# Kernel tuning notes

Hardware: AMD Instinct MI355X
Metric: run time of the kernel (lower is better)

## Reference

```python
import jax, jax.numpy as jnp
import numpy as np

T, D, E, I, TOP_K = 4096, 2048, 8, 4096, 2

def setup_inputs() -> dict:
    key = jax.random.key(0)
    k1, k2, k3, k4, k5 = jax.random.split(key, 5)
    s = 0.02
    return {
        "hidden_states": jax.random.normal(k1, (T, D), jnp.float32),
        "wr": jax.random.normal(k2, (E, D), jnp.float32) * s,
        "w1": jax.random.normal(k3, (E, I, D), jnp.float32) * s,
        "v1": jax.random.normal(k4, (E, I, D), jnp.float32) * s,
        "w2": jax.random.normal(k5, (E, D, I), jnp.float32) * s,
        "index": 0,
    }

def reference(hidden_states, wr, w1, v1, w2, index):
    # index selects the layer; n_layers == 1 here so weights are already that layer's.
    x = hidden_states.reshape(-1, D)  # [T, D]
    # Router logits + softmax top-k with renormalization (fused_moe semantics)
    logits = x @ wr.T                                  # [T, E]
    probs = jax.nn.softmax(logits, axis=-1)
    topw, topi = jax.lax.top_k(probs, TOP_K)           # [T, K]
    topw = topw / jnp.sum(topw, axis=-1, keepdims=True)
    # Dense per-token gate matrix, zero for non-selected experts
    t_idx = jnp.arange(x.shape[0])[:, None]
    gates = jnp.zeros((x.shape[0], E), x.dtype).at[t_idx, topi].set(topw)  # [T, E]
    # SiLU-GLU experts: (silu(x w1^T) * (x v1^T)) w2^T, combined by gates
    out = jnp.zeros_like(x)
    for e in range(E):  # fixed small expert count
        h = jax.nn.silu(x @ w1[e].T) * (x @ v1[e].T)   # [T, I]
        out = out + gates[:, e:e + 1] * (h @ w2[e].T)  # [T, D]
    return out
```

## Files before the change

### kernel.cpp

```cpp
#include <hip/hip_runtime.h>
#include <hip/hip_bf16.h>
#include <cstdint>


#define T_TOK 4096
#define DHID  2048
#define NEXP  8
#define IDIM  4096
#define NSLOT (T_TOK * 2)

#define BM 128
#define BN 128
#define BK 64

typedef __bf16 bf16x8 __attribute__((ext_vector_type(8)));
typedef float  f32x4  __attribute__((ext_vector_type(4)));

__global__ __launch_bounds__(64) void router_kernel(
    const float* __restrict__ x, const float* __restrict__ wr,
    __bf16* __restrict__ xb, int* __restrict__ topi, float* __restrict__ topg,
    int* __restrict__ cnt)
{
    int t = blockIdx.x;
    int lane = threadIdx.x;
    const float* xr = x + (size_t)t * DHID;
    float acc[NEXP];
#pragma unroll
    for (int e = 0; e < NEXP; ++e) acc[e] = 0.f;
    for (int j = 0; j < DHID / 64; ++j) {
        int d = lane + j * 64;
        float xv = xr[d];
        xb[(size_t)t * DHID + d] = (__bf16)xv;
#pragma unroll
        for (int e = 0; e < NEXP; ++e) acc[e] += xv * wr[e * DHID + d];
    }
#pragma unroll
    for (int e = 0; e < NEXP; ++e) {
#pragma unroll
        for (int s = 32; s > 0; s >>= 1) acc[e] += __shfl_xor(acc[e], s);
    }
    if (lane == 0) {
        int e0 = 0; float l0 = acc[0];
#pragma unroll
        for (int e = 1; e < NEXP; ++e) if (acc[e] > l0) { l0 = acc[e]; e0 = e; }
        int e1 = -1; float l1 = -3.4e38f;
#pragma unroll
        for (int e = 0; e < NEXP; ++e) if (e != e0 && acc[e] > l1) { l1 = acc[e]; e1 = e; }
        float g0 = 1.f / (1.f + __expf(l1 - l0));
        topi[t * 2]     = e0; topi[t * 2 + 1] = e1;
        topg[t * 2]     = g0; topg[t * 2 + 1] = 1.f - g0;
        atomicAdd(&cnt[e0], 1); atomicAdd(&cnt[e1], 1);
    }
}

__global__ void scan_kernel(const int* __restrict__ cnt, int* __restrict__ basep,
                            int* __restrict__ fill)
{
    if (threadIdx.x == 0 && blockIdx.x == 0) {
        int s = 0;
#pragma unroll
        for (int e = 0; e < NEXP; ++e) { basep[e] = s; s += cnt[e]; fill[e] = 0; }
    }
}

__global__ __launch_bounds__(256) void assign_kernel(
    const int* __restrict__ topi, const float* __restrict__ topg,
    const int* __restrict__ basep, int* __restrict__ fill,
    int* __restrict__ tok_of_slot, float* __restrict__ gate_of_slot,
    int* __restrict__ slot_of)
{
    int t = blockIdx.x * 256 + threadIdx.x;
    if (t >= T_TOK) return;
#pragma unroll
    for (int k = 0; k < 2; ++k) {
        int e = topi[t * 2 + k];
        int slot = basep[e] + atomicAdd(&fill[e], 1);
        tok_of_slot[slot] = t;
        gate_of_slot[slot] = topg[t * 2 + k];
        slot_of[t * 2 + k] = slot;
    }
}

__global__ __launch_bounds__(256, 2) void gemm1_kernel(
    const __bf16* __restrict__ xb, const float* __restrict__ w1,
    const float* __restrict__ v1, const int* __restrict__ tok_of_slot,
    const int* __restrict__ cnt, const int* __restrict__ basep,
    __bf16* __restrict__ H)
{
    int e  = blockIdx.z;
    int ne = cnt[e];
    int m0 = blockIdx.y * BM;
    if (m0 >= ne) return;
    int n0 = blockIdx.x * BN;
    int sbase = basep[e] + m0;

    __shared__ __bf16 As[BM * BK];
    __shared__ __bf16 B1s[BN * BK];
    __shared__ __bf16 B2s[BN * BK];
    __shared__ int toks[BM];

    int tid = threadIdx.x;
    if (tid < BM) {
        int t = 0;
        if (m0 + tid < ne) t = tok_of_slot[sbase + tid];
        toks[tid] = t;
    }
    __syncthreads();

    const float* w1e = w1 + (size_t)e * IDIM * DHID;
    const float* v1e = v1 + (size_t)e * IDIM * DHID;

    int lane = tid & 63;
    int wave = tid >> 6;
    int wr0 = (wave >> 1) * 64;
    int wc0 = (wave & 1) * 64;

    f32x4 acc1[4][4], acc2[4][4];
    f32x4 zf = {0.f, 0.f, 0.f, 0.f};
#pragma unroll
    for (int m = 0; m < 4; ++m)
#pragma unroll
        for (int n = 0; n < 4; ++n) { acc1[m][n] = zf; acc2[m][n] = zf; }

    char* AsB = (char*)As;
    char* B1B = (char*)B1s;
    char* B2B = (char*)B2s;

    int row0 = tid >> 3;
    int ch   = tid & 7;
    int g    = row0 & 7;
    const __bf16* a_src[4];
    const float*  b1_src[4];
    const float*  b2_src[4];
    int dstoff[4];
#pragma unroll
    for (int p = 0; p < 4; ++p) {
        int row = row0 + 32 * p;
        a_src[p]  = xb  + (size_t)toks[row] * DHID + ch * 8;
        b1_src[p] = w1e + (size_t)(n0 + row) * DHID + ch * 8;
        b2_src[p] = v1e + (size_t)(n0 + row) * DHID + ch * 8;
        dstoff[p] = row * 128 + ((ch * 16) ^ (g << 4));
    }

    for (int k0 = 0; k0 < DHID; k0 += BK) {
#pragma unroll
        for (int p = 0; p < 4; ++p)
            *(uint4*)(AsB + dstoff[p]) = *(const uint4*)(a_src[p] + k0);
#pragma unroll
        for (int p = 0; p < 4; ++p) {
            float4 fa = *(const float4*)(b1_src[p] + k0);
            float4 fb = *(const float4*)(b1_src[p] + k0 + 4);
            bf16x8 bv;
            bv[0]=(__bf16)fa.x; bv[1]=(__bf16)fa.y; bv[2]=(__bf16)fa.z; bv[3]=(__bf16)fa.w;
            bv[4]=(__bf16)fb.x; bv[5]=(__bf16)fb.y; bv[6]=(__bf16)fb.z; bv[7]=(__bf16)fb.w;
            *(bf16x8*)(B1B + dstoff[p]) = bv;
        }
#pragma unroll
        for (int p = 0; p < 4; ++p) {
            float4 fa = *(const float4*)(b2_src[p] + k0);
            float4 fb = *(const float4*)(b2_src[p] + k0 + 4);
            bf16x8 bv;
            bv[0]=(__bf16)fa.x; bv[1]=(__bf16)fa.y; bv[2]=(__bf16)fa.z; bv[3]=(__bf16)fa.w;
            bv[4]=(__bf16)fb.x; bv[5]=(__bf16)fb.y; bv[6]=(__bf16)fb.z; bv[7]=(__bf16)fb.w;
            *(bf16x8*)(B2B + dstoff[p]) = bv;
        }
        __syncthreads();
#pragma unroll
        for (int ks = 0; ks < 2; ++ks) {
            int kb = ks * 64 + (lane >> 4) * 16;
            bf16x8 af[4], b1f[4], b2f[4];
#pragma unroll
            for (int m = 0; m < 4; ++m) {
                int row = wr0 + m * 16 + (lane & 15);
                af[m] = *(const bf16x8*)(AsB + row * 128 + (kb ^ ((row & 7) << 4)));
            }
#pragma unroll
            for (int n = 0; n < 4; ++n) {
                int row = wc0 + n * 16 + (lane & 15);
                int off = row * 128 + (kb ^ ((row & 7) << 4));
                b1f[n] = *(const bf16x8*)(B1B + off);
                b2f[n] = *(const bf16x8*)(B2B + off);
            }
#pragma unroll
            for (int m = 0; m < 4; ++m)
#pragma unroll
                for (int n = 0; n < 4; ++n) {
                    acc1[m][n] = __builtin_amdgcn_mfma_f32_16x16x32_bf16(af[m], b1f[n], acc1[m][n], 0, 0, 0);
                    acc2[m][n] = __builtin_amdgcn_mfma_f32_16x16x32_bf16(af[m], b2f[n], acc2[m][n], 0, 0, 0);
                }
        }
        __syncthreads();
    }

#pragma unroll
    for (int m = 0; m < 4; ++m) {
        int rbase = wr0 + m * 16 + ((lane >> 4) * 4);
#pragma unroll
        for (int n = 0; n < 4; ++n) {
            int col = n0 + wc0 + n * 16 + (lane & 15);
#pragma unroll
            for (int r = 0; r < 4; ++r) {
                int lrow = rbase + r;
                if (m0 + lrow < ne) {
                    float a = acc1[m][n][r];
                    float b = acc2[m][n][r];
                    float h = (a / (1.f + __expf(-a))) * b;
                    H[(size_t)(sbase + lrow) * IDIM + col] = (__bf16)h;
                }
            }
        }
    }
}

__global__ __launch_bounds__(256, 2) void gemm2_kernel(
    const __bf16* __restrict__ H, const float* __restrict__ w2,
    const float* __restrict__ gate_of_slot, const int* __restrict__ cnt,
    const int* __restrict__ basep, __bf16* __restrict__ outslot)
{
    int e  = blockIdx.z;
    int ne = cnt[e];
    int m0 = blockIdx.y * BM;
    if (m0 >= ne) return;
    int n0 = blockIdx.x * BN;
    int sbase = basep[e] + m0;

    __shared__ __bf16 As[BM * BK];
    __shared__ __bf16 Bs[BN * BK];
    __shared__ float gates[BM];

    int tid = threadIdx.x;
    if (tid < BM) {
        int srow = sbase + tid;
        if (m0 + tid >= ne) srow = sbase;
        gates[tid] = gate_of_slot[srow];
    }

    const float* w2e = w2 + (size_t)e * DHID * IDIM;

    int lane = tid & 63;
    int wave = tid >> 6;
    int wr0 = (wave >> 1) * 64;
    int wc0 = (wave & 1) * 64;

    f32x4 acc[4][4];
    f32x4 zf = {0.f, 0.f, 0.f, 0.f};
#pragma unroll
    for (int m = 0; m < 4; ++m)
#pragma unroll
        for (int n = 0; n < 4; ++n) acc[m][n] = zf;

    char* AsB = (char*)As;
    char* BsB = (char*)Bs;

    int row0 = tid >> 3;
    int ch   = tid & 7;
    int g    = row0 & 7;
    const __bf16* a_src[4];
    const float*  b_src[4];
    int dstoff[4];
#pragma unroll
    for (int p = 0; p < 4; ++p) {
        int row = row0 + 32 * p;
        int srow = sbase + row;
        if (m0 + row >= ne) srow = sbase;
        a_src[p]  = H   + (size_t)srow * IDIM + ch * 8;
        b_src[p]  = w2e + (size_t)(n0 + row) * IDIM + ch * 8;
        dstoff[p] = row * 128 + ((ch * 16) ^ (g << 4));
    }

    for (int k0 = 0; k0 < IDIM; k0 += BK) {
#pragma unroll
        for (int p = 0; p < 4; ++p)
            *(uint4*)(AsB + dstoff[p]) = *(const uint4*)(a_src[p] + k0);
#pragma unroll
        for (int p = 0; p < 4; ++p) {
            float4 fa = *(const float4*)(b_src[p] + k0);
            float4 fb = *(const float4*)(b_src[p] + k0 + 4);
            bf16x8 bv;
            bv[0]=(__bf16)fa.x; bv[1]=(__bf16)fa.y; bv[2]=(__bf16)fa.z; bv[3]=(__bf16)fa.w;
            bv[4]=(__bf16)fb.x; bv[5]=(__bf16)fb.y; bv[6]=(__bf16)fb.z; bv[7]=(__bf16)fb.w;
            *(bf16x8*)(BsB + dstoff[p]) = bv;
        }
        __syncthreads();
#pragma unroll
        for (int ks = 0; ks < 2; ++ks) {
            int kb = ks * 64 + (lane >> 4) * 16;
            bf16x8 af[4], bf[4];
#pragma unroll
            for (int m = 0; m < 4; ++m) {
                int row = wr0 + m * 16 + (lane & 15);
                af[m] = *(const bf16x8*)(AsB + row * 128 + (kb ^ ((row & 7) << 4)));
            }
#pragma unroll
            for (int n = 0; n < 4; ++n) {
                int row = wc0 + n * 16 + (lane & 15);
                bf[n] = *(const bf16x8*)(BsB + row * 128 + (kb ^ ((row & 7) << 4)));
            }
#pragma unroll
            for (int m = 0; m < 4; ++m)
#pragma unroll
                for (int n = 0; n < 4; ++n)
                    acc[m][n] = __builtin_amdgcn_mfma_f32_16x16x32_bf16(af[m], bf[n], acc[m][n], 0, 0, 0);
        }
        __syncthreads();
    }

#pragma unroll
    for (int m = 0; m < 4; ++m) {
        int rbase = wr0 + m * 16 + ((lane >> 4) * 4);
#pragma unroll
        for (int n = 0; n < 4; ++n) {
            int col = n0 + wc0 + n * 16 + (lane & 15);
#pragma unroll
            for (int r = 0; r < 4; ++r) {
                int lrow = rbase + r;
                if (m0 + lrow < ne) {
                    float v = acc[m][n][r] * gates[lrow];
                    outslot[(size_t)(sbase + lrow) * DHID + col] = (__bf16)v;
                }
            }
        }
    }
}

__global__ __launch_bounds__(256) void combine_kernel(
    const __bf16* __restrict__ outslot, const int* __restrict__ slot_of,
    float* __restrict__ out)
{
    int idx = blockIdx.x * 256 + threadIdx.x;
    int t = idx >> 8;
    int c = (idx & 255) * 8;
    int s0 = slot_of[t * 2], s1 = slot_of[t * 2 + 1];
    bf16x8 a = *(const bf16x8*)(outslot + (size_t)s0 * DHID + c);
    bf16x8 b = *(const bf16x8*)(outslot + (size_t)s1 * DHID + c);
    float4 o0, o1;
    o0.x = (float)a[0] + (float)b[0];
    o0.y = (float)a[1] + (float)b[1];
    o0.z = (float)a[2] + (float)b[2];
    o0.w = (float)a[3] + (float)b[3];
    o1.x = (float)a[4] + (float)b[4];
    o1.y = (float)a[5] + (float)b[5];
    o1.z = (float)a[6] + (float)b[6];
    o1.w = (float)a[7] + (float)b[7];
    *(float4*)(out + (size_t)t * DHID + c)     = o0;
    *(float4*)(out + (size_t)t * DHID + c + 4) = o1;
}

extern "C" void kernel_launch(void* const* d_in, const int* in_sizes, int n_in,
                              void* d_out, int out_size, void* d_ws, size_t ws_size,
                              hipStream_t stream)
{
    (void)in_sizes; (void)n_in; (void)out_size; (void)ws_size;
    const float* x  = (const float*)d_in[0];
    const float* wr = (const float*)d_in[1];
    const float* w1 = (const float*)d_in[2];
    const float* v1 = (const float*)d_in[3];
    const float* w2 = (const float*)d_in[4];
    float* out = (float*)d_out;

    char* ws = (char*)d_ws;
    size_t off = 0;
    auto alloc = [&](size_t bytes) -> void* {
        void* p = ws + off;
        off += bytes;
        off = (off + 255) & ~(size_t)255;
        return p;
    };
    __bf16* xb       = (__bf16*)alloc((size_t)T_TOK * DHID * 2);
    __bf16* H        = (__bf16*)alloc((size_t)NSLOT * IDIM * 2);
    __bf16* outslot  = (__bf16*)alloc((size_t)NSLOT * DHID * 2);
    int*    topi     = (int*)  alloc((size_t)T_TOK * 2 * 4);
    float*  topg     = (float*)alloc((size_t)T_TOK * 2 * 4);
    int*    tok_of_slot  = (int*)  alloc((size_t)NSLOT * 4);
    float*  gate_of_slot = (float*)alloc((size_t)NSLOT * 4);
    int*    slot_of  = (int*)  alloc((size_t)NSLOT * 4);
    int*    cnt      = (int*)  alloc(NEXP * 4);
    int*    basep    = (int*)  alloc(NEXP * 4);
    int*    fill     = (int*)  alloc(NEXP * 4);

    hipMemsetAsync(cnt, 0, NEXP * 4, stream);
    router_kernel<<<T_TOK, 64, 0, stream>>>(x, wr, xb, topi, topg, cnt);
    scan_kernel<<<1, 64, 0, stream>>>(cnt, basep, fill);
    assign_kernel<<<T_TOK / 256, 256, 0, stream>>>(topi, topg, basep, fill,
                                                   tok_of_slot, gate_of_slot, slot_of);
    gemm1_kernel<<<dim3(IDIM / BN, T_TOK / BM, NEXP), 256, 0, stream>>>(
        xb, w1, v1, tok_of_slot, cnt, basep, H);
    gemm2_kernel<<<dim3(DHID / BN, T_TOK / BM, NEXP), 256, 0, stream>>>(
        H, w2, gate_of_slot, cnt, basep, outslot);
    combine_kernel<<<(T_TOK * DHID / 8) / 256, 256, 0, stream>>>(outslot, slot_of, out);
}
```

Before: 877.3 us.

## Unify MoE GEMMs into a double-buffered template with direct-to-LDS loads

Replaces the separate gate/up and down GEMM kernels with one templated kernel that double-buffers the LDS tiles, loads activation tiles with global_load_lds, and prefetches fp32 weights into registers for the next K step. The fused gate/up GEMM is split into two passes: the first writes silu(x·w1) to H1 and the second multiplies in x·v1 elementwise in place. This halves per-block register and LDS pressure, but the activation is read twice and H1 makes an extra round trip through global memory. The router also now handles four tokens per block with float4 loads.

```diff
diff --git a/kernel.cpp b/kernel.cpp
--- a/kernel.cpp
+++ b/kernel.cpp
@@ -14,25 +14,40 @@
 #define BK 64
 
 typedef __bf16 bf16x8 __attribute__((ext_vector_type(8)));
+typedef __bf16 bf16x4 __attribute__((ext_vector_type(4)));
 typedef float  f32x4  __attribute__((ext_vector_type(4)));
 
-__global__ __launch_bounds__(64) void router_kernel(
+__device__ __forceinline__ void gload_lds16(const void* g, void* l) {
+    __builtin_amdgcn_global_load_lds(
+        (const __attribute__((address_space(1))) uint32_t*)g,
+        (__attribute__((address_space(3))) uint32_t*)l, 16, 0, 0);
+}
+
+__global__ __launch_bounds__(256) void router_kernel(
     const float* __restrict__ x, const float* __restrict__ wr,
     __bf16* __restrict__ xb, int* __restrict__ topi, float* __restrict__ topg,
     int* __restrict__ cnt)
 {
-    int t = blockIdx.x;
-    int lane = threadIdx.x;
-    const float* xr = x + (size_t)t * DHID;
+    int wave = threadIdx.x >> 6, lane = threadIdx.x & 63;
+    int t = blockIdx.x * 4 + wave;
+    const float4* xr = (const float4*)(x + (size_t)t * DHID);
+    bf16x4* xbo = (bf16x4*)(xb + (size_t)t * DHID);
     float acc[NEXP];
 #pragma unroll
     for (int e = 0; e < NEXP; ++e) acc[e] = 0.f;
-    for (int j = 0; j < DHID / 64; ++j) {
-        int d = lane + j * 64;
-        float xv = xr[d];
-        xb[(size_t)t * DHID + d] = (__bf16)xv;
-#pragma unroll
-        for (int e = 0; e < NEXP; ++e) acc[e] += xv * wr[e * DHID + d];
+#pragma unroll
+    for (int j = 0; j < DHID / 256; ++j) {
+        int d4 = lane + j * 64;
+        float4 v = xr[d4];
+        bf16x4 bv;
+        bv[0] = (__bf16)v.x; bv[1] = (__bf16)v.y;
+        bv[2] = (__bf16)v.z; bv[3] = (__bf16)v.w;
+        xbo[d4] = bv;
+#pragma unroll
+        for (int e = 0; e < NEXP; ++e) {
+            float4 w = ((const float4*)(wr + e * DHID))[d4];
+            acc[e] += v.x * w.x + v.y * w.y + v.z * w.z + v.w * w.w;
+        }
     }
 #pragma unroll
     for (int e = 0; e < NEXP; ++e) {
@@ -47,8 +62,8 @@
 #pragma unroll
         for (int e = 0; e < NEXP; ++e) if (e != e0 && acc[e] > l1) { l1 = acc[e]; e1 = e; }
         float g0 = 1.f / (1.f + __expf(l1 - l0));
-        topi[t * 2]     = e0; topi[t * 2 + 1] = e1;
-        topg[t * 2]     = g0; topg[t * 2 + 1] = 1.f - g0;
+        topi[t * 2] = e0; topi[t * 2 + 1] = e1;
+        topg[t * 2] = g0; topg[t * 2 + 1] = 1.f - g0;
         atomicAdd(&cnt[e0], 1); atomicAdd(&cnt[e1], 1);
     }
 }
@@ -81,11 +96,12 @@
     }
 }
 
-__global__ __launch_bounds__(256, 2) void gemm1_kernel(
-    const __bf16* __restrict__ xb, const float* __restrict__ w1,
-    const float* __restrict__ v1, const int* __restrict__ tok_of_slot,
+template <int PASS, int KDIM, int NDIM>
+__global__ __launch_bounds__(256, 2) void moe_gemm(
+    const __bf16* __restrict__ Abase, const float* __restrict__ W,
+    const int* __restrict__ tok_of_slot, const float* __restrict__ gate_of_slot,
     const int* __restrict__ cnt, const int* __restrict__ basep,
-    __bf16* __restrict__ H)
+    __bf16* Out, const __bf16* H1r)
 {
     int e  = blockIdx.z;
     int ne = cnt[e];
@@ -94,102 +110,118 @@
     int n0 = blockIdx.x * BN;
     int sbase = basep[e] + m0;
 
-    __shared__ __bf16 As[BM * BK];
-    __shared__ __bf16 B1s[BN * BK];
-    __shared__ __bf16 B2s[BN * BK];
-    __shared__ int toks[BM];
+    __shared__ __bf16 As[2][BM * BK];
+    __shared__ __bf16 Bs[2][BN * BK];
+    __shared__ int   toks[BM];
+    __shared__ float gates[BM];
 
     int tid = threadIdx.x;
-    if (tid < BM) {
-        int t = 0;
-        if (m0 + tid < ne) t = tok_of_slot[sbase + tid];
-        toks[tid] = t;
+    if (PASS < 3) {
+        if (tid < BM) toks[tid] = (m0 + tid < ne) ? tok_of_slot[sbase + tid] : 0;
+    } else {
+        if (tid < BM) gates[tid] = gate_of_slot[(m0 + tid < ne) ? (sbase + tid) : sbase];
     }
     __syncthreads();
 
-    const float* w1e = w1 + (size_t)e * IDIM * DHID;
-    const float* v1e = v1 + (size_t)e * IDIM * DHID;
-
-    int lane = tid & 63;
-    int wave = tid >> 6;
-    int wr0 = (wave >> 1) * 64;
-    int wc0 = (wave & 1) * 64;
-
-    f32x4 acc1[4][4], acc2[4][4];
-    f32x4 zf = {0.f, 0.f, 0.f, 0.f};
-#pragma unroll
-    for (int m = 0; m < 4; ++m)
-#pragma unroll
-        for (int n = 0; n < 4; ++n) { acc1[m][n] = zf; acc2[m][n] = zf; }
-
-    char* AsB = (char*)As;
-    char* B1B = (char*)B1s;
-    char* B2B = (char*)B2s;
-
-    int row0 = tid >> 3;
-    int ch   = tid & 7;
-    int g    = row0 & 7;
+    const float* We = W + (size_t)e * NDIM * KDIM;
+    int lane = tid & 63, wave = tid >> 6;
+    int wr0 = (wave >> 1) * 64, wc0 = (wave & 1) * 64;
+
+    char* AsB = (char*)&As[0][0];
+    char* BsB = (char*)&Bs[0][0];
+
     const __bf16* a_src[4];
-    const float*  b1_src[4];
-    const float*  b2_src[4];
+    char* a_dst[4];
+    {
+        int p = lane & 7;
+#pragma unroll
+        for (int j = 0; j < 4; ++j) {
+            int chunk = wave * 4 + j;
+            int arow  = chunk * 8 + (lane >> 3);
+            int csw   = p ^ (arow & 7);
+            size_t grow;
+            if (PASS < 3) {
+                grow = (size_t)toks[arow] * DHID;
+            } else {
+                int srow = (m0 + arow < ne) ? (sbase + arow) : sbase;
+                grow = (size_t)srow * KDIM;
+            }
+            a_src[j] = Abase + grow + csw * 8;
+            a_dst[j] = AsB + chunk * 1024;
+        }
+    }
+    int row0 = tid >> 3, ch = tid & 7;
+    const float* b_src[4];
     int dstoff[4];
 #pragma unroll
     for (int p = 0; p < 4; ++p) {
         int row = row0 + 32 * p;
-        a_src[p]  = xb  + (size_t)toks[row] * DHID + ch * 8;
-        b1_src[p] = w1e + (size_t)(n0 + row) * DHID + ch * 8;
-        b2_src[p] = v1e + (size_t)(n0 + row) * DHID + ch * 8;
-        dstoff[p] = row * 128 + ((ch * 16) ^ (g << 4));
-    }
-
-    for (int k0 = 0; k0 < DHID; k0 += BK) {
-#pragma unroll
-        for (int p = 0; p < 4; ++p)
-            *(uint4*)(AsB + dstoff[p]) = *(const uint4*)(a_src[p] + k0);
+        b_src[p] = We + (size_t)(n0 + row) * KDIM + ch * 8;
+        dstoff[p] = row * 128 + ((ch * 16) ^ ((row & 7) << 4));
+    }
+
+    f32x4 acc[4][4];
+    f32x4 zf = {0.f, 0.f, 0.f, 0.f};
+#pragma unroll
+    for (int m = 0; m < 4; ++m)
+#pragma unroll
+        for (int n = 0; n < 4; ++n) acc[m][n] = zf;
+
+    float4 pb[8];
+
+#pragma unroll
+    for (int j = 0; j < 4; ++j) gload_lds16(a_src[j], a_dst[j]);
+#pragma unroll
+    for (int p = 0; p < 4; ++p) {
+        pb[2 * p]     = *(const float4*)(b_src[p]);
+        pb[2 * p + 1] = *(const float4*)(b_src[p] + 4);
+    }
+
+    const int NK = KDIM / BK;
+    for (int kt = 0; kt < NK; ++kt) {
+        int cur = kt & 1;
 #pragma unroll
         for (int p = 0; p < 4; ++p) {
-            float4 fa = *(const float4*)(b1_src[p] + k0);
-            float4 fb = *(const float4*)(b1_src[p] + k0 + 4);
+            float4 fa = pb[2 * p], fb = pb[2 * p + 1];
             bf16x8 bv;
             bv[0]=(__bf16)fa.x; bv[1]=(__bf16)fa.y; bv[2]=(__bf16)fa.z; bv[3]=(__bf16)fa.w;
             bv[4]=(__bf16)fb.x; bv[5]=(__bf16)fb.y; bv[6]=(__bf16)fb.z; bv[7]=(__bf16)fb.w;
-            *(bf16x8*)(B1B + dstoff[p]) = bv;
-        }
-#pragma unroll
-        for (int p = 0; p < 4; ++p) {
-            float4 fa = *(const float4*)(b2_src[p] + k0);
-            float4 fb = *(const float4*)(b2_src[p] + k0 + 4);
-            bf16x8 bv;
-            bv[0]=(__bf16)fa.x; bv[1]=(__bf16)fa.y; bv[2]=(__bf16)fa.z; bv[3]=(__bf16)fa.w;
-            bv[4]=(__bf16)fb.x; bv[5]=(__bf16)fb.y; bv[6]=(__bf16)fb.z; bv[7]=(__bf16)fb.w;
-            *(bf16x8*)(B2B + dstoff[p]) = bv;
+            *(bf16x8*)(BsB + cur * 16384 + dstoff[p]) = bv;
         }
         __syncthreads();
+        if (kt + 1 < NK) {
+            int nxt = cur ^ 1;
+            int koff = (kt + 1) * BK;
+#pragma unroll
+            for (int j = 0; j < 4; ++j)
+                gload_lds16(a_src[j] + koff, a_dst[j] + nxt * 16384);
+#pragma unroll
+            for (int p = 0; p < 4; ++p) {
+                pb[2 * p]     = *(const float4*)(b_src[p] + koff);
+                pb[2 * p + 1] = *(const float4*)(b_src[p] + koff + 4);
+            }
+        }
 #pragma unroll
         for (int ks = 0; ks < 2; ++ks) {
-            int kb = ks * 64 + (lane >> 4) * 16;
-            bf16x8 af[4], b1f[4], b2f[4];
+            bf16x8 af[4], bfr[4];
 #pragma unroll
             for (int m = 0; m < 4; ++m) {
                 int row = wr0 + m * 16 + (lane & 15);
-                af[m] = *(const bf16x8*)(AsB + row * 128 + (kb ^ ((row & 7) << 4)));
+                af[m] = *(const bf16x8*)(AsB + cur * 16384 + row * 128 +
+                                         ((ks * 64 + (lane >> 4) * 16) ^ ((row & 7) << 4)));
             }
 #pragma unroll
             for (int n = 0; n < 4; ++n) {
                 int row = wc0 + n * 16 + (lane & 15);
-                int off = row * 128 + (kb ^ ((row & 7) << 4));
-                b1f[n] = *(const bf16x8*)(B1B + off);
-                b2f[n] = *(const bf16x8*)(B2B + off);
+                bfr[n] = *(const bf16x8*)(BsB + cur * 16384 + row * 128 +
+                                          ((ks * 64 + (lane >> 4) * 16) ^ ((row & 7) << 4)));
             }
 #pragma unroll
             for (int m = 0; m < 4; ++m)
 #pragma unroll
-                for (int n = 0; n < 4; ++n) {
-                    acc1[m][n] = __builtin_amdgcn_mfma_f32_16x16x32_bf16(af[m], b1f[n], acc1[m][n], 0, 0, 0);
-                    acc2[m][n] = __builtin_amdgcn_mfma_f32_16x16x32_bf16(af[m], b2f[n], acc2[m][n], 0, 0, 0);
-                }
-        }
-        __syncthreads();
+                for (int n = 0; n < 4; ++n)
+                    acc[m][n] = __builtin_amdgcn_mfma_f32_16x16x32_bf16(af[m], bfr[n], acc[m][n], 0, 0, 0);
+        }
     }
 
 #pragma unroll
@@ -202,121 +234,16 @@
             for (int r = 0; r < 4; ++r) {
                 int lrow = rbase + r;
                 if (m0 + lrow < ne) {
-                    float a = acc1[m][n][r];
-                    float b = acc2[m][n][r];
-                    float h = (a / (1.f + __expf(-a))) * b;
-                    H[(size_t)(sbase + lrow) * IDIM + col] = (__bf16)h;
-                }
-            }
-        }
-    }
-}
-
-__global__ __launch_bounds__(256, 2) void gemm2_kernel(
-    const __bf16* __restrict__ H, const float* __restrict__ w2,
-    const float* __restrict__ gate_of_slot, const int* __restrict__ cnt,
-    const int* __restrict__ basep, __bf16* __restrict__ outslot)
-{
-    int e  = blockIdx.z;
-    int ne = cnt[e];
-    int m0 = blockIdx.y * BM;
-    if (m0 >= ne) return;
-    int n0 = blockIdx.x * BN;
-    int sbase = basep[e] + m0;
-
-    __shared__ __bf16 As[BM * BK];
-    __shared__ __bf16 Bs[BN * BK];
-    __shared__ float gates[BM];
-
-    int tid = threadIdx.x;
-    if (tid < BM) {
-        int srow = sbase + tid;
-        if (m0 + tid >= ne) srow = sbase;
-        gates[tid] = gate_of_slot[srow];
-    }
-
-    const float* w2e = w2 + (size_t)e * DHID * IDIM;
-
-    int lane = tid & 63;
-    int wave = tid >> 6;
-    int wr0 = (wave >> 1) * 64;
-    int wc0 = (wave & 1) * 64;
-
-    f32x4 acc[4][4];
-    f32x4 zf = {0.f, 0.f, 0.f, 0.f};
-#pragma unroll
-    for (int m = 0; m < 4; ++m)
-#pragma unroll
-        for (int n = 0; n < 4; ++n) acc[m][n] = zf;
-
-    char* AsB = (char*)As;
-    char* BsB = (char*)Bs;
-
-    int row0 = tid >> 3;
-    int ch   = tid & 7;
-    int g    = row0 & 7;
-    const __bf16* a_src[4];
-    const float*  b_src[4];
-    int dstoff[4];
-#pragma unroll
-    for (int p = 0; p < 4; ++p) {
-        int row = row0 + 32 * p;
-        int srow = sbase + row;
-        if (m0 + row >= ne) srow = sbase;
-        a_src[p]  = H   + (size_t)srow * IDIM + ch * 8;
-        b_src[p]  = w2e + (size_t)(n0 + row) * IDIM + ch * 8;
-        dstoff[p] = row * 128 + ((ch * 16) ^ (g << 4));
-    }
-
-    for (int k0 = 0; k0 < IDIM; k0 += BK) {
-#pragma unroll
-        for (int p = 0; p < 4; ++p)
-            *(uint4*)(AsB + dstoff[p]) = *(const uint4*)(a_src[p] + k0);
-#pragma unroll
-        for (int p = 0; p < 4; ++p) {
-            float4 fa = *(const float4*)(b_src[p] + k0);
-            float4 fb = *(const float4*)(b_src[p] + k0 + 4);
-            bf16x8 bv;
-            bv[0]=(__bf16)fa.x; bv[1]=(__bf16)fa.y; bv[2]=(__bf16)fa.z; bv[3]=(__bf16)fa.w;
-            bv[4]=(__bf16)fb.x; bv[5]=(__bf16)fb.y; bv[6]=(__bf16)fb.z; bv[7]=(__bf16)fb.w;
-            *(bf16x8*)(BsB + dstoff[p]) = bv;
-        }
-        __syncthreads();
-#pragma unroll
-        for (int ks = 0; ks < 2; ++ks) {
-            int kb = ks * 64 + (lane >> 4) * 16;
-            bf16x8 af[4], bf[4];
-#pragma unroll
-            for (int m = 0; m < 4; ++m) {
-                int row = wr0 + m * 16 + (lane & 15);
-                af[m] = *(const bf16x8*)(AsB + row * 128 + (kb ^ ((row & 7) << 4)));
-            }
-#pragma unroll
-            for (int n = 0; n < 4; ++n) {
-                int row = wc0 + n * 16 + (lane & 15);
-                bf[n] = *(const bf16x8*)(BsB + row * 128 + (kb ^ ((row & 7) << 4)));
-            }
-#pragma unroll
-            for (int m = 0; m < 4; ++m)
-#pragma unroll
-                for (int n = 0; n < 4; ++n)
-                    acc[m][n] = __builtin_amdgcn_mfma_f32_16x16x32_bf16(af[m], bf[n], acc[m][n], 0, 0, 0);
-        }
-        __syncthreads();
-    }
-
-#pragma unroll
-    for (int m = 0; m < 4; ++m) {
-        int rbase = wr0 + m * 16 + ((lane >> 4) * 4);
-#pragma unroll
-        for (int n = 0; n < 4; ++n) {
-            int col = n0 + wc0 + n * 16 + (lane & 15);
-#pragma unroll
-            for (int r = 0; r < 4; ++r) {
-                int lrow = rbase + r;
-                if (m0 + lrow < ne) {
-                    float v = acc[m][n][r] * gates[lrow];
-                    outslot[(size_t)(sbase + lrow) * DHID + col] = (__bf16)v;
+                    size_t oidx = (size_t)(sbase + lrow) * NDIM + col;
+                    float v = acc[m][n][r];
+                    if (PASS == 1) {
+                        v = v / (1.f + __expf(-v));
+                    } else if (PASS == 2) {
+                        v = (float)H1r[oidx] * v;
+                    } else {
+                        v = v * gates[lrow];
+                    }
+                    Out[oidx] = (__bf16)v;
                 }
             }
         }
@@ -366,26 +293,28 @@
         off = (off + 255) & ~(size_t)255;
         return p;
     };
-    __bf16* xb       = (__bf16*)alloc((size_t)T_TOK * DHID * 2);
-    __bf16* H        = (__bf16*)alloc((size_t)NSLOT * IDIM * 2);
-    __bf16* outslot  = (__bf16*)alloc((size_t)NSLOT * DHID * 2);
-    int*    topi     = (int*)  alloc((size_t)T_TOK * 2 * 4);
-    float*  topg     = (float*)alloc((size_t)T_TOK * 2 * 4);
+    __bf16* xb      = (__bf16*)alloc((size_t)T_TOK * DHID * 2);
+    __bf16* H1      = (__bf16*)alloc((size_t)NSLOT * IDIM * 2);
+    __bf16* outslot = (__bf16*)alloc((size_t)NSLOT * DHID * 2);
+    int*    topi    = (int*)  alloc((size_t)T_TOK * 2 * 4);
+    float*  topg    = (float*)alloc((size_t)T_TOK * 2 * 4);
     int*    tok_of_slot  = (int*)  alloc((size_t)NSLOT * 4);
     float*  gate_of_slot = (float*)alloc((size_t)NSLOT * 4);
-    int*    slot_of  = (int*)  alloc((size_t)NSLOT * 4);
-    int*    cnt      = (int*)  alloc(NEXP * 4);
-    int*    basep    = (int*)  alloc(NEXP * 4);
-    int*    fill     = (int*)  alloc(NEXP * 4);
+    int*    slot_of = (int*)  alloc((size_t)NSLOT * 4);
+    int*    cnt     = (int*)  alloc(NEXP * 4);
+    int*    basep   = (int*)  alloc(NEXP * 4);
+    int*    fill    = (int*)  alloc(NEXP * 4);
 
     hipMemsetAsync(cnt, 0, NEXP * 4, stream);
-    router_kernel<<<T_TOK, 64, 0, stream>>>(x, wr, xb, topi, topg, cnt);
+    router_kernel<<<T_TOK / 4, 256, 0, stream>>>(x, wr, xb, topi, topg, cnt);
     scan_kernel<<<1, 64, 0, stream>>>(cnt, basep, fill);
     assign_kernel<<<T_TOK / 256, 256, 0, stream>>>(topi, topg, basep, fill,
                                                    tok_of_slot, gate_of_slot, slot_of);
-    gemm1_kernel<<<dim3(IDIM / BN, T_TOK / BM, NEXP), 256, 0, stream>>>(
-        xb, w1, v1, tok_of_slot, cnt, basep, H);
-    gemm2_kernel<<<dim3(DHID / BN, T_TOK / BM, NEXP), 256, 0, stream>>>(
-        H, w2, gate_of_slot, cnt, basep, outslot);
+    moe_gemm<1, DHID, IDIM><<<dim3(IDIM / BN, T_TOK / BM, NEXP), 256, 0, stream>>>(
+        xb, w1, tok_of_slot, gate_of_slot, cnt, basep, H1, nullptr);
+    moe_gemm<2, DHID, IDIM><<<dim3(IDIM / BN, T_TOK / BM, NEXP), 256, 0, stream>>>(
+        xb, v1, tok_of_slot, gate_of_slot, cnt, basep, H1, H1);
+    moe_gemm<3, IDIM, DHID><<<dim3(DHID / BN, T_TOK / BM, NEXP), 256, 0, stream>>>(
+        H1, w2, tok_of_slot, gate_of_slot, cnt, basep, outslot, nullptr);
     combine_kernel<<<(T_TOK * DHID / 8) / 256, 256, 0, stream>>>(outslot, slot_of, out);
 }
```

Measured after the change: 1.363 ms. 55.4% more time.
